# Optimization experiments

Measured on AMD Instinct MI355X. Metric: run time of the kernel, lower is better.

Reference implementation:

```python
import jax, jax.numpy as jnp
import numpy as np

NUM_HEADS = 16

def setup_inputs() -> dict:
    key = jax.random.key(0)
    k1, k2, k3 = jax.random.split(key, 3)
    B, N, D = 2, 2048, 1024
    x = jax.random.normal(k1, (B, N, D), dtype=jnp.float32)
    w_qkv = jax.random.normal(k2, (D, 3 * D), dtype=jnp.float32) * (D ** -0.5)
    w_out = jax.random.normal(k3, (D, D), dtype=jnp.float32) * (D ** -0.5)
    return {"x": x, "w_qkv": w_qkv, "w_out": w_out}

def reference(x, w_qkv, w_out):
    B, N, D = x.shape
    H = NUM_HEADS
    d = D // H
    scale = d ** -0.5
    qkv = x @ w_qkv  # [B, N, 3D]
    q, k, v = jnp.split(qkv, 3, axis=-1)
    # b n (h d) -> b h n d
    split_heads = lambda t: t.reshape(B, N, H, d).transpose(0, 2, 1, 3)
    q, k, v = split_heads(q), split_heads(k), split_heads(v)
    dots = jnp.einsum('bhid,bhjd->bhij', q, k) * scale
    # causal mask: -inf above the diagonal
    causal = jnp.tril(jnp.ones((N, N), dtype=bool))
    dots = jnp.where(causal, dots, jnp.float32(-jnp.inf))
    attn = jax.nn.softmax(dots, axis=-1)
    out = jnp.einsum('bhij,bhjd->bhid', attn, v)
    out = out.transpose(0, 2, 1, 3).reshape(B, N, D)  # b h n d -> b n (h d)
    return out @ w_out
```

## Files before the change

### kernel.cpp

```cpp
#include <hip/hip_runtime.h>


typedef __bf16 bf16x8 __attribute__((ext_vector_type(8)));
typedef float f32x4 __attribute__((ext_vector_type(4)));

#define MFMA16(a, b, c) __builtin_amdgcn_mfma_f32_16x16x32_bf16((a), (b), (c), 0, 0, 0)

#define LDS_FENCE()                                   \
  do {                                                \
    asm volatile("s_waitcnt lgkmcnt(0)" ::: "memory");\
    __builtin_amdgcn_sched_barrier(0);                \
  } while (0)
#define LDS_ORDER() asm volatile("" ::: "memory")

#define MAX3(a, b, c) fmaxf(fmaxf((a), (b)), (c))

__device__ __forceinline__ unsigned short f2bf(float f) {
  __bf16 h = (__bf16)f;
  return *(unsigned short*)&h;
}

__global__ __launch_bounds__(256) void prep_kernel(
    const float* __restrict__ x, const float* __restrict__ wqkv,
    const float* __restrict__ wout, unsigned short* __restrict__ xb,
    unsigned short* __restrict__ wqkvT, unsigned short* __restrict__ woutT) {
  __shared__ float tile[32][33];
  const int id = blockIdx.x, t = threadIdx.x;
  if (id < 4096) {
    const int i = id * 256 + t;
    float4 v = ((const float4*)x)[i];
    ushort4 o;
    o.x = f2bf(v.x); o.y = f2bf(v.y); o.z = f2bf(v.z); o.w = f2bf(v.w);
    ((ushort4*)xb)[i] = o;
    return;
  }
  const int tx = t & 31, ty = t >> 5;
  const float* in; unsigned short* out;
  int C, scale_rows, bx, by;
  if (id < 7168) {
    const int q = id - 4096;
    in = wqkv; out = wqkvT; C = 3072; scale_rows = 1024;
    bx = q % 96; by = q / 96;
  } else {
    const int q = id - 7168;
    in = wout; out = woutT; C = 1024; scale_rows = 0;
    bx = q & 31; by = q >> 5;
  }
#pragma unroll
  for (int i = ty; i < 32; i += 8)
    tile[i][tx] = in[(size_t)(by * 32 + i) * C + bx * 32 + tx];
  __syncthreads();
#pragma unroll
  for (int i = ty; i < 32; i += 8) {
    const int orow = bx * 32 + i;
    const float s = (orow < scale_rows) ? 0.18033688f : 1.0f;
    out[(size_t)orow * 1024 + by * 32 + tx] = f2bf(tile[tx][i] * s);
  }
}

__global__ void transpose_v_kernel(const unsigned short* __restrict__ qkv,
                                   unsigned short* __restrict__ vT) {
  __shared__ unsigned short tile[32][33];
  const int b = blockIdx.z, bx = blockIdx.x, by = blockIdx.y;
  const int tx = threadIdx.x, ty = threadIdx.y;
#pragma unroll
  for (int i = ty; i < 32; i += 8)
    tile[i][tx] = qkv[(size_t)(b * 2048 + by * 32 + i) * 3072 + 2048 + bx * 32 + tx];
  __syncthreads();
#pragma unroll
  for (int i = ty; i < 32; i += 8)
    vT[((size_t)b * 1024 + bx * 32 + i) * 2048 + by * 32 + tx] = tile[tx][i];
}

template <int OUT_BF16>
__global__ __launch_bounds__(256) void gemm128_kernel(
    const unsigned short* __restrict__ A,
    const unsigned short* __restrict__ BT,
    void* __restrict__ Cp, int M, int Nc, int K) {
  __shared__ unsigned short lA[128 * 32];
  __shared__ unsigned short lB[128 * 32];
  const int t = threadIdx.x;
  const int l = t & 63, g = l >> 4, c = l & 15;
  const int w = t >> 6;
  const int wm = (w >> 1) * 64, wn = (w & 1) * 64;
  const int bm = blockIdx.y * 128, bn = blockIdx.x * 128;

  const int i0 = t, i1 = 256 + t;
  const unsigned short* ga0 = A + (size_t)(bm + (i0 >> 2)) * K + (i0 & 3) * 8;
  const unsigned short* ga1 = A + (size_t)(bm + (i1 >> 2)) * K + (i1 & 3) * 8;
  const unsigned short* gb0 = BT + (size_t)(bn + (i0 >> 2)) * K + (i0 & 3) * 8;
  const unsigned short* gb1 = BT + (size_t)(bn + (i1 >> 2)) * K + (i1 & 3) * 8;
  unsigned short* la0 = lA + (i0 & ~63) * 8;
  unsigned short* la1 = lA + (i1 & ~63) * 8;
  unsigned short* lb0 = lB + (i0 & ~63) * 8;
  unsigned short* lb1 = lB + (i1 & ~63) * 8;

  f32x4 acc[4][4] = {};

  for (int kk = 0; kk < K; kk += 32) {
    __syncthreads();
    __builtin_amdgcn_global_load_lds(
        (const __attribute__((address_space(1))) void*)(ga0 + kk),
        (__attribute__((address_space(3))) void*)la0, 16, 0, 0);
    __builtin_amdgcn_global_load_lds(
        (const __attribute__((address_space(1))) void*)(ga1 + kk),
        (__attribute__((address_space(3))) void*)la1, 16, 0, 0);
    __builtin_amdgcn_global_load_lds(
        (const __attribute__((address_space(1))) void*)(gb0 + kk),
        (__attribute__((address_space(3))) void*)lb0, 16, 0, 0);
    __builtin_amdgcn_global_load_lds(
        (const __attribute__((address_space(1))) void*)(gb1 + kk),
        (__attribute__((address_space(3))) void*)lb1, 16, 0, 0);
    __syncthreads();

    bf16x8 af[4], bfr[4];
#pragma unroll
    for (int mi = 0; mi < 4; ++mi)
      af[mi] = *(const bf16x8*)(lA + (wm + mi * 16 + c) * 32 + g * 8);
#pragma unroll
    for (int ni = 0; ni < 4; ++ni)
      bfr[ni] = *(const bf16x8*)(lB + (wn + ni * 16 + c) * 32 + g * 8);
#pragma unroll
    for (int mi = 0; mi < 4; ++mi)
#pragma unroll
      for (int ni = 0; ni < 4; ++ni)
        acc[mi][ni] = MFMA16(af[mi], bfr[ni], acc[mi][ni]);
  }

  if (OUT_BF16) {
    unsigned short* Cc = (unsigned short*)Cp;
#pragma unroll
    for (int mi = 0; mi < 4; ++mi)
#pragma unroll
      for (int r = 0; r < 4; ++r) {
        const int gr = bm + wm + mi * 16 + g * 4 + r;
#pragma unroll
        for (int ni = 0; ni < 4; ++ni)
          Cc[(size_t)gr * Nc + bn + wn + ni * 16 + c] = f2bf(acc[mi][ni][r]);
      }
  } else {
    float* Cf = (float*)Cp;
#pragma unroll
    for (int mi = 0; mi < 4; ++mi)
#pragma unroll
      for (int r = 0; r < 4; ++r) {
        const int gr = bm + wm + mi * 16 + g * 4 + r;
#pragma unroll
        for (int ni = 0; ni < 4; ++ni)
          Cf[(size_t)gr * Nc + bn + wn + ni * 16 + c] = acc[mi][ni][r];
      }
  }
}

__global__ __launch_bounds__(256) void attn_kernel(
    const unsigned short* __restrict__ qkv,
    const unsigned short* __restrict__ vT,
    unsigned short* __restrict__ aout) {
  const int t = threadIdx.x, w = t >> 6, l = t & 63, g = l >> 4, c = l & 15;
  const int g4 = g * 4, c7 = c & 7;

  const int id0 = blockIdx.x;
  const int xcd = id0 & 7, pos = id0 >> 3;
  const int bh = xcd * 4 + (pos & 3);
  const int tile = 31 - (pos >> 2);
  const int b = bh >> 4, h = bh & 15;

  __shared__ __align__(16) unsigned short lK[2][64][64];
  __shared__ __align__(16) unsigned short lV[2][64][64];
  __shared__ __align__(16) unsigned short pl[4][16][40];

  const unsigned short* Qbase = qkv + (size_t)b * 2048 * 3072 + h * 64;
  const unsigned short* Kb = Qbase + 1024;
  const unsigned short* Vb = vT + ((size_t)b * 1024 + h * 64) * 2048;

#define KFRAG(row, half) (*(const bf16x8*)(Kb + (size_t)(row) * 3072 + (half) * 32 + g * 8))
#define VFRAG(dt, kvoff) (*(const bf16x8*)(Vb + (size_t)((dt) * 16 + c) * 2048 + (kvoff) + g * 8))

#define STAGE(dK, dV, kb_)                                                    \
  do {                                                                        \
    _Pragma("unroll")                                                         \
    for (int q = 0; q < 2; ++q) {                                             \
      const int idx = q * 256 + t;                                            \
      const int row = idx >> 3, ch = idx & 7;                                 \
      const int sc = (ch ^ (row & 7)) * 8;                                    \
      __builtin_amdgcn_global_load_lds(                                       \
          (const __attribute__((address_space(1))) void*)(                    \
              Kb + (size_t)(kb_ + row) * 3072 + sc),                          \
          (__attribute__((address_space(3))) void*)(                          \
              &(dK)[0][0] + (idx & ~63) * 8), 16, 0, 0);                      \
      __builtin_amdgcn_global_load_lds(                                       \
          (const __attribute__((address_space(1))) void*)(                    \
              Vb + (size_t)row * 2048 + (kb_) + sc),                          \
          (__attribute__((address_space(3))) void*)(                          \
              &(dV)[0][0] + (idx & ~63) * 8), 16, 0, 0);                      \
    }                                                                         \
  } while (0)

  const int q0 = tile * 64 + w * 16;
  const int qc = q0 + c;

  const bf16x8 bq0 = *(const bf16x8*)(Qbase + (size_t)qc * 3072 + g * 8);
  const bf16x8 bq1 = *(const bf16x8*)(Qbase + (size_t)qc * 3072 + 32 + g * 8);

  f32x4 o[4] = {};
  float m_c = -__builtin_inff(), llp = 0.f;

  if (tile > 0) {
    STAGE(lK[0], lV[0], 0);
    int cur = 0;
#pragma unroll 1
    for (int jb = 0; jb < tile; ++jb) {
      __syncthreads();
      if (jb + 1 < tile) STAGE(lK[cur ^ 1], lV[cur ^ 1], (jb + 1) * 64);

      const unsigned short* lk = &lK[cur][0][0];
      const unsigned short* lv = &lV[cur][0][0];

      bf16x8 ka[8];
#pragma unroll
      for (int n = 0; n < 4; ++n) {
        ka[2 * n]     = *(const bf16x8*)(lk + (16 * n + c) * 64 + ((g ^ c7) * 8));
        ka[2 * n + 1] = *(const bf16x8*)(lk + (16 * n + c) * 64 + (((4 + g) ^ c7) * 8));
      }
      bf16x8 bv[2][4];
#pragma unroll
      for (int ks = 0; ks < 2; ++ks)
#pragma unroll
        for (int dt = 0; dt < 4; ++dt)
          bv[ks][dt] = *(const bf16x8*)(lv + (dt * 16 + c) * 64 + (((ks * 4 + g) ^ c7) * 8));

      f32x4 s[4] = {};
      __builtin_amdgcn_s_setprio(1);
#pragma unroll
      for (int n = 0; n < 4; ++n) {
        s[n] = MFMA16(ka[2 * n], bq0, s[n]);
        s[n] = MFMA16(ka[2 * n + 1], bq1, s[n]);
      }
      __builtin_amdgcn_s_setprio(0);

      const float t0 = MAX3(s[0][0], s[0][1], s[0][2]);
      const float t1 = MAX3(s[0][3], s[1][0], s[1][1]);
      const float t2 = MAX3(s[1][2], s[1][3], s[2][0]);
      const float t3 = MAX3(s[2][1], s[2][2], s[2][3]);
      const float t4 = MAX3(s[3][0], s[3][1], s[3][2]);
      const float vml = fmaxf(MAX3(t0, t1, t2), MAX3(t3, t4, s[3][3]));

      if (!__all(vml - m_c <= 5.0f)) {
        float vm = vml;
        vm = fmaxf(vm, __shfl_xor(vm, 16));
        vm = fmaxf(vm, __shfl_xor(vm, 32));
        const float mn = fmaxf(m_c, vm);
        const float al = exp2f(m_c - mn);
        m_c = mn;
        llp *= al;
#pragma unroll
        for (int r = 0; r < 4; ++r) {
          const float alr = __shfl(al, g4 + r);
          o[0][r] *= alr; o[1][r] *= alr; o[2][r] *= alr; o[3][r] *= alr;
        }
      }

#pragma unroll
      for (int n = 0; n < 4; ++n)
#pragma unroll
        for (int r = 0; r < 4; ++r)
          s[n][r] = exp2f(s[n][r] - m_c);

      llp += ((s[0][0] + s[0][1]) + (s[0][2] + s[0][3])) +
             ((s[1][0] + s[1][1]) + (s[1][2] + s[1][3])) +
             ((s[2][0] + s[2][1]) + (s[2][2] + s[2][3])) +
             ((s[3][0] + s[3][1]) + (s[3][2] + s[3][3]));

      LDS_ORDER();
#pragma unroll
      for (int n = 0; n < 2; ++n) {
        ushort4 pw;
        pw.x = f2bf(s[n][0]); pw.y = f2bf(s[n][1]);
        pw.z = f2bf(s[n][2]); pw.w = f2bf(s[n][3]);
        *(ushort4*)&pl[w][c][n * 16 + g4] = pw;
      }
      LDS_FENCE();
      const bf16x8 pa0 = *(const bf16x8*)&pl[w][c][g * 8];
      LDS_FENCE();
#pragma unroll
      for (int n = 2; n < 4; ++n) {
        ushort4 pw;
        pw.x = f2bf(s[n][0]); pw.y = f2bf(s[n][1]);
        pw.z = f2bf(s[n][2]); pw.w = f2bf(s[n][3]);
        *(ushort4*)&pl[w][c][(n - 2) * 16 + g4] = pw;
      }
      LDS_FENCE();
      const bf16x8 pa1 = *(const bf16x8*)&pl[w][c][g * 8];

      __builtin_amdgcn_s_setprio(1);
#pragma unroll
      for (int dt = 0; dt < 4; ++dt) {
        o[dt] = MFMA16(pa0, bv[0][dt], o[dt]);
        o[dt] = MFMA16(pa1, bv[1][dt], o[dt]);
      }
      __builtin_amdgcn_s_setprio(0);
      cur ^= 1;
    }
  }

  const int ndiag = 1 + (w >> 1);
#pragma unroll 1
  for (int j = 0; j < ndiag; ++j) {
    const int kb = tile * 64 + j * 32;
    const bf16x8 k00 = KFRAG(kb + c, 0), k01 = KFRAG(kb + c, 1);
    const bf16x8 k10 = KFRAG(kb + 16 + c, 0), k11 = KFRAG(kb + 16 + c, 1);
    const bf16x8 bv0 = VFRAG(0, kb), bv1 = VFRAG(1, kb);
    const bf16x8 bv2 = VFRAG(2, kb), bv3 = VFRAG(3, kb);

    f32x4 s0 = {}, s1 = {};
    s0 = MFMA16(k00, bq0, s0);
    s0 = MFMA16(k01, bq1, s0);
    s1 = MFMA16(k10, bq0, s1);
    s1 = MFMA16(k11, bq1, s1);

    float v0[4], v1[4];
#pragma unroll
    for (int r = 0; r < 4; ++r) {
      v0[r] = (kb + g4 + r <= qc) ? s0[r] : -__builtin_inff();
      v1[r] = (kb + 16 + g4 + r <= qc) ? s1[r] : -__builtin_inff();
    }
    const float t0 = MAX3(v0[0], v0[1], v0[2]);
    const float t1 = MAX3(v0[3], v1[0], v1[1]);
    const float vml = fmaxf(fmaxf(t0, t1), fmaxf(v1[2], v1[3]));
    if (!__all(vml - m_c <= 5.0f)) {
      float vm = vml;
      vm = fmaxf(vm, __shfl_xor(vm, 16));
      vm = fmaxf(vm, __shfl_xor(vm, 32));
      const float mn = fmaxf(m_c, vm);
      const float al = exp2f(m_c - mn);
      m_c = mn;
      llp *= al;
#pragma unroll
      for (int r = 0; r < 4; ++r) {
        const float alr = __shfl(al, g4 + r);
        o[0][r] *= alr; o[1][r] *= alr; o[2][r] *= alr; o[3][r] *= alr;
      }
    }
    float p0[4], p1[4];
#pragma unroll
    for (int r = 0; r < 4; ++r) {
      p0[r] = exp2f(v0[r] - m_c);
      p1[r] = exp2f(v1[r] - m_c);
    }
    llp += ((p0[0] + p0[1]) + (p0[2] + p0[3])) +
           ((p1[0] + p1[1]) + (p1[2] + p1[3]));

    LDS_ORDER();
    ushort4 pw;
    pw.x = f2bf(p0[0]); pw.y = f2bf(p0[1]); pw.z = f2bf(p0[2]); pw.w = f2bf(p0[3]);
    *(ushort4*)&pl[w][c][g4] = pw;
    pw.x = f2bf(p1[0]); pw.y = f2bf(p1[1]); pw.z = f2bf(p1[2]); pw.w = f2bf(p1[3]);
    *(ushort4*)&pl[w][c][16 + g4] = pw;
    LDS_FENCE();
    const bf16x8 pa = *(const bf16x8*)&pl[w][c][g * 8];

    o[0] = MFMA16(pa, bv0, o[0]);
    o[1] = MFMA16(pa, bv1, o[1]);
    o[2] = MFMA16(pa, bv2, o[2]);
    o[3] = MFMA16(pa, bv3, o[3]);
  }

  float ll = llp;
  ll += __shfl_xor(ll, 16);
  ll += __shfl_xor(ll, 32);
  const float inv = 1.0f / ll;
#pragma unroll
  for (int r = 0; r < 4; ++r) {
    const float invr = __shfl(inv, g4 + r);
    const size_t row = (size_t)(b * 2048 + q0 + g4 + r);
#pragma unroll
    for (int dt = 0; dt < 4; ++dt)
      aout[row * 1024 + h * 64 + dt * 16 + c] = f2bf(o[dt][r] * invr);
  }
#undef KFRAG
#undef VFRAG
#undef STAGE
}

extern "C" void kernel_launch(void* const* d_in, const int* in_sizes, int n_in,
                              void* d_out, int out_size, void* d_ws, size_t ws_size,
                              hipStream_t stream) {
  const float* x = (const float*)d_in[0];
  const float* wqkv = (const float*)d_in[1];
  const float* wout = (const float*)d_in[2];
  float* out = (float*)d_out;

  unsigned short* ws = (unsigned short*)d_ws;
  unsigned short* xb = ws;
  unsigned short* wqkvT = xb + (size_t)4096 * 1024;
  unsigned short* woutT = wqkvT + (size_t)3072 * 1024;
  unsigned short* qkv = woutT + (size_t)1024 * 1024;
  unsigned short* vT = qkv + (size_t)4096 * 3072;
  unsigned short* aout = vT + (size_t)2 * 1024 * 2048;

  prep_kernel<<<8192, 256, 0, stream>>>(x, wqkv, wout, xb, wqkvT, woutT);
  gemm128_kernel<1><<<dim3(24, 32), 256, 0, stream>>>(xb, wqkvT, qkv, 4096, 3072, 1024);
  transpose_v_kernel<<<dim3(32, 64, 2), dim3(32, 8), 0, stream>>>(qkv, vT);
  attn_kernel<<<1024, 256, 0, stream>>>(qkv, vT, aout);
  gemm128_kernel<0><<<dim3(8, 32), 256, 0, stream>>>(aout, woutT, out, 4096, 1024, 1024);
}
```

Measured before the change: 132.8 us.

## Switch attention to 32x32 MFMA with register-shuffled P fragments and 2-wave blocks

Rewrites the attention kernel to use 32x32x16 bf16 MFMA tiles, with each of two waves per block owning 32 query rows instead of four waves owning 16. The P matrix is converted to bf16 with packed conversions and rearranged through cross-lane shuffles rather than a round trip through LDS with wait fences. The diagonal blocks are also handled per wave with 32-wide chunks. This cuts LDS traffic and synchronisation for P and raises MFMA efficiency, but it halves the threads per block, doubles per-thread accumulator and register pressure, and doubles each thread's staging load share.

Result: slower. 152.7 us (+15.0%).

```diff
diff --git a/kernel.cpp b/kernel.cpp
--- a/kernel.cpp
+++ b/kernel.cpp
@@ -3,22 +3,36 @@
 
 typedef __bf16 bf16x8 __attribute__((ext_vector_type(8)));
 typedef float f32x4 __attribute__((ext_vector_type(4)));
+typedef float f32x16 __attribute__((ext_vector_type(16)));
+typedef unsigned int uint4v __attribute__((ext_vector_type(4)));
 
 #define MFMA16(a, b, c) __builtin_amdgcn_mfma_f32_16x16x32_bf16((a), (b), (c), 0, 0, 0)
-
-#define LDS_FENCE()                                   \
-  do {                                                \
-    asm volatile("s_waitcnt lgkmcnt(0)" ::: "memory");\
-    __builtin_amdgcn_sched_barrier(0);                \
-  } while (0)
-#define LDS_ORDER() asm volatile("" ::: "memory")
-
-#define MAX3(a, b, c) fmaxf(fmaxf((a), (b)), (c))
+#define MFMA32(a, b, c) __builtin_amdgcn_mfma_f32_32x32x16_bf16((a), (b), (c), 0, 0, 0)
 
 __device__ __forceinline__ unsigned short f2bf(float f) {
   __bf16 h = (__bf16)f;
   return *(unsigned short*)&h;
 }
+
+__device__ __forceinline__ unsigned cvtpk_bf16(float lo, float hi) {
+  unsigned r;
+  asm("v_cvt_pk_bf16_f32 %0, %1, %2" : "=v"(r) : "v"(lo), "v"(hi));
+  return r;
+}
+
+#define PFRAG(dst, sv, base)                                   \
+  do {                                                         \
+    const unsigned X0 = cvtpk_bf16((sv)[(base) + 0], (sv)[(base) + 1]); \
+    const unsigned X1 = cvtpk_bf16((sv)[(base) + 2], (sv)[(base) + 3]); \
+    const unsigned Y0 = cvtpk_bf16((sv)[(base) + 4], (sv)[(base) + 5]); \
+    const unsigned Y1 = cvtpk_bf16((sv)[(base) + 6], (sv)[(base) + 7]); \
+    const unsigned c0 = __shfl_xor(hi ? X0 : Y0, 32);          \
+    const unsigned c1 = __shfl_xor(hi ? X1 : Y1, 32);          \
+    uint4v u;                                                  \
+    u.x = hi ? c0 : X0; u.y = hi ? c1 : X1;                    \
+    u.z = hi ? Y0 : c0; u.w = hi ? Y1 : c1;                    \
+    dst = __builtin_bit_cast(bf16x8, u);                       \
+  } while (0)
 
 __global__ __launch_bounds__(256) void prep_kernel(
     const float* __restrict__ x, const float* __restrict__ wqkv,
@@ -152,35 +166,36 @@
   }
 }
 
-__global__ __launch_bounds__(256) void attn_kernel(
+__global__ __launch_bounds__(128, 2) void attn_kernel(
     const unsigned short* __restrict__ qkv,
     const unsigned short* __restrict__ vT,
     unsigned short* __restrict__ aout) {
-  const int t = threadIdx.x, w = t >> 6, l = t & 63, g = l >> 4, c = l & 15;
-  const int g4 = g * 4, c7 = c & 7;
+  const int t = threadIdx.x;
+  const int w = t >> 6;
+  const int l = t & 63;
+  const int col = l & 31;
+  const int hi = l >> 5;
+  const int hi4 = hi * 4;
+  const int c7 = col & 7;
 
   const int id0 = blockIdx.x;
   const int xcd = id0 & 7, pos = id0 >> 3;
   const int bh = xcd * 4 + (pos & 3);
-  const int tile = 31 - (pos >> 2);
+  const int T = 31 - (pos >> 2);
   const int b = bh >> 4, h = bh & 15;
 
   __shared__ __align__(16) unsigned short lK[2][64][64];
   __shared__ __align__(16) unsigned short lV[2][64][64];
-  __shared__ __align__(16) unsigned short pl[4][16][40];
 
   const unsigned short* Qbase = qkv + (size_t)b * 2048 * 3072 + h * 64;
   const unsigned short* Kb = Qbase + 1024;
   const unsigned short* Vb = vT + ((size_t)b * 1024 + h * 64) * 2048;
 
-#define KFRAG(row, half) (*(const bf16x8*)(Kb + (size_t)(row) * 3072 + (half) * 32 + g * 8))
-#define VFRAG(dt, kvoff) (*(const bf16x8*)(Vb + (size_t)((dt) * 16 + c) * 2048 + (kvoff) + g * 8))
-
 #define STAGE(dK, dV, kb_)                                                    \
   do {                                                                        \
     _Pragma("unroll")                                                         \
-    for (int q = 0; q < 2; ++q) {                                             \
-      const int idx = q * 256 + t;                                            \
+    for (int qq = 0; qq < 4; ++qq) {                                          \
+      const int idx = qq * 128 + t;                                           \
       const int row = idx >> 3, ch = idx & 7;                                 \
       const int sc = (ch ^ (row & 7)) * 8;                                    \
       __builtin_amdgcn_global_load_lds(                                       \
@@ -196,189 +211,165 @@
     }                                                                         \
   } while (0)
 
-  const int q0 = tile * 64 + w * 16;
-  const int qc = q0 + c;
-
-  const bf16x8 bq0 = *(const bf16x8*)(Qbase + (size_t)qc * 3072 + g * 8);
-  const bf16x8 bq1 = *(const bf16x8*)(Qbase + (size_t)qc * 3072 + 32 + g * 8);
-
-  f32x4 o[4] = {};
+  const int q0w = T * 64 + w * 32;
+  const int qg = q0w + col;
+
+  bf16x8 bq[4];
+#pragma unroll
+  for (int c16 = 0; c16 < 4; ++c16)
+    bq[c16] = *(const bf16x8*)(Qbase + (size_t)qg * 3072 + c16 * 16 + hi * 8);
+
+  f32x16 o0 = {}, o1 = {};
   float m_c = -__builtin_inff(), llp = 0.f;
 
-  if (tile > 0) {
+  if (T > 0) {
     STAGE(lK[0], lV[0], 0);
     int cur = 0;
 #pragma unroll 1
-    for (int jb = 0; jb < tile; ++jb) {
+    for (int jb = 0; jb < T; ++jb) {
       __syncthreads();
-      if (jb + 1 < tile) STAGE(lK[cur ^ 1], lV[cur ^ 1], (jb + 1) * 64);
+      if (jb + 1 < T) STAGE(lK[cur ^ 1], lV[cur ^ 1], (jb + 1) * 64);
 
       const unsigned short* lk = &lK[cur][0][0];
       const unsigned short* lv = &lV[cur][0][0];
 
-      bf16x8 ka[8];
-#pragma unroll
-      for (int n = 0; n < 4; ++n) {
-        ka[2 * n]     = *(const bf16x8*)(lk + (16 * n + c) * 64 + ((g ^ c7) * 8));
-        ka[2 * n + 1] = *(const bf16x8*)(lk + (16 * n + c) * 64 + (((4 + g) ^ c7) * 8));
-      }
-      bf16x8 bv[2][4];
-#pragma unroll
-      for (int ks = 0; ks < 2; ++ks)
-#pragma unroll
-        for (int dt = 0; dt < 4; ++dt)
-          bv[ks][dt] = *(const bf16x8*)(lv + (dt * 16 + c) * 64 + (((ks * 4 + g) ^ c7) * 8));
-
-      f32x4 s[4] = {};
+      f32x16 s0 = {}, s1 = {};
       __builtin_amdgcn_s_setprio(1);
 #pragma unroll
-      for (int n = 0; n < 4; ++n) {
-        s[n] = MFMA16(ka[2 * n], bq0, s[n]);
-        s[n] = MFMA16(ka[2 * n + 1], bq1, s[n]);
+      for (int c16 = 0; c16 < 4; ++c16) {
+        const int chl = c16 * 2 + hi;
+        const bf16x8 k0 = *(const bf16x8*)(lk + (col)*64 + ((chl ^ c7) * 8));
+        const bf16x8 k1 = *(const bf16x8*)(lk + (32 + col) * 64 + ((chl ^ c7) * 8));
+        s0 = MFMA32(k0, bq[c16], s0);
+        s1 = MFMA32(k1, bq[c16], s1);
       }
       __builtin_amdgcn_s_setprio(0);
 
-      const float t0 = MAX3(s[0][0], s[0][1], s[0][2]);
-      const float t1 = MAX3(s[0][3], s[1][0], s[1][1]);
-      const float t2 = MAX3(s[1][2], s[1][3], s[2][0]);
-      const float t3 = MAX3(s[2][1], s[2][2], s[2][3]);
-      const float t4 = MAX3(s[3][0], s[3][1], s[3][2]);
-      const float vml = fmaxf(MAX3(t0, t1, t2), MAX3(t3, t4, s[3][3]));
+      float a[16];
+#pragma unroll
+      for (int i = 0; i < 16; ++i) a[i] = fmaxf(s0[i], s1[i]);
+#pragma unroll
+      for (int kk = 8; kk; kk >>= 1)
+#pragma unroll
+        for (int i = 0; i < kk; ++i) a[i] = fmaxf(a[i], a[i + kk]);
+      const float vml = fmaxf(a[0], __shfl_xor(a[0], 32));
 
       if (!__all(vml - m_c <= 5.0f)) {
-        float vm = vml;
-        vm = fmaxf(vm, __shfl_xor(vm, 16));
-        vm = fmaxf(vm, __shfl_xor(vm, 32));
-        const float mn = fmaxf(m_c, vm);
+        const float mn = fmaxf(m_c, vml);
         const float al = exp2f(m_c - mn);
-        m_c = mn;
-        llp *= al;
-#pragma unroll
-        for (int r = 0; r < 4; ++r) {
-          const float alr = __shfl(al, g4 + r);
-          o[0][r] *= alr; o[1][r] *= alr; o[2][r] *= alr; o[3][r] *= alr;
+        m_c = mn; llp *= al;
+#pragma unroll
+        for (int r = 0; r < 16; ++r) {
+          const float alr = __shfl(al, (r & 3) + 8 * (r >> 2) + hi4);
+          o0[r] *= alr; o1[r] *= alr;
         }
       }
 
 #pragma unroll
-      for (int n = 0; n < 4; ++n)
-#pragma unroll
-        for (int r = 0; r < 4; ++r)
-          s[n][r] = exp2f(s[n][r] - m_c);
-
-      llp += ((s[0][0] + s[0][1]) + (s[0][2] + s[0][3])) +
-             ((s[1][0] + s[1][1]) + (s[1][2] + s[1][3])) +
-             ((s[2][0] + s[2][1]) + (s[2][2] + s[2][3])) +
-             ((s[3][0] + s[3][1]) + (s[3][2] + s[3][3]));
-
-      LDS_ORDER();
-#pragma unroll
-      for (int n = 0; n < 2; ++n) {
-        ushort4 pw;
-        pw.x = f2bf(s[n][0]); pw.y = f2bf(s[n][1]);
-        pw.z = f2bf(s[n][2]); pw.w = f2bf(s[n][3]);
-        *(ushort4*)&pl[w][c][n * 16 + g4] = pw;
-      }
-      LDS_FENCE();
-      const bf16x8 pa0 = *(const bf16x8*)&pl[w][c][g * 8];
-      LDS_FENCE();
-#pragma unroll
-      for (int n = 2; n < 4; ++n) {
-        ushort4 pw;
-        pw.x = f2bf(s[n][0]); pw.y = f2bf(s[n][1]);
-        pw.z = f2bf(s[n][2]); pw.w = f2bf(s[n][3]);
-        *(ushort4*)&pl[w][c][(n - 2) * 16 + g4] = pw;
-      }
-      LDS_FENCE();
-      const bf16x8 pa1 = *(const bf16x8*)&pl[w][c][g * 8];
+      for (int i = 0; i < 16; ++i) {
+        s0[i] = exp2f(s0[i] - m_c);
+        s1[i] = exp2f(s1[i] - m_c);
+      }
+      float sm[16];
+#pragma unroll
+      for (int i = 0; i < 16; ++i) sm[i] = s0[i] + s1[i];
+#pragma unroll
+      for (int kk = 8; kk; kk >>= 1)
+#pragma unroll
+        for (int i = 0; i < kk; ++i) sm[i] += sm[i + kk];
+      llp += sm[0];
+
+      bf16x8 pf0, pf1, pf2, pf3;
+      PFRAG(pf0, s0, 0); PFRAG(pf1, s0, 8);
+      PFRAG(pf2, s1, 0); PFRAG(pf3, s1, 8);
 
       __builtin_amdgcn_s_setprio(1);
 #pragma unroll
-      for (int dt = 0; dt < 4; ++dt) {
-        o[dt] = MFMA16(pa0, bv[0][dt], o[dt]);
-        o[dt] = MFMA16(pa1, bv[1][dt], o[dt]);
+      for (int ck = 0; ck < 4; ++ck) {
+        const int chl = ck * 2 + hi;
+        const bf16x8 v0 = *(const bf16x8*)(lv + (col)*64 + ((chl ^ c7) * 8));
+        const bf16x8 v1 = *(const bf16x8*)(lv + (32 + col) * 64 + ((chl ^ c7) * 8));
+        const bf16x8 pf = (ck == 0) ? pf0 : (ck == 1) ? pf1 : (ck == 2) ? pf2 : pf3;
+        o0 = MFMA32(pf, v0, o0);
+        o1 = MFMA32(pf, v1, o1);
       }
       __builtin_amdgcn_s_setprio(0);
       cur ^= 1;
     }
   }
 
-  const int ndiag = 1 + (w >> 1);
-#pragma unroll 1
-  for (int j = 0; j < ndiag; ++j) {
-    const int kb = tile * 64 + j * 32;
-    const bf16x8 k00 = KFRAG(kb + c, 0), k01 = KFRAG(kb + c, 1);
-    const bf16x8 k10 = KFRAG(kb + 16 + c, 0), k11 = KFRAG(kb + 16 + c, 1);
-    const bf16x8 bv0 = VFRAG(0, kb), bv1 = VFRAG(1, kb);
-    const bf16x8 bv2 = VFRAG(2, kb), bv3 = VFRAG(3, kb);
-
-    f32x4 s0 = {}, s1 = {};
-    s0 = MFMA16(k00, bq0, s0);
-    s0 = MFMA16(k01, bq1, s0);
-    s1 = MFMA16(k10, bq0, s1);
-    s1 = MFMA16(k11, bq1, s1);
-
-    float v0[4], v1[4];
-#pragma unroll
-    for (int r = 0; r < 4; ++r) {
-      v0[r] = (kb + g4 + r <= qc) ? s0[r] : -__builtin_inff();
-      v1[r] = (kb + 16 + g4 + r <= qc) ? s1[r] : -__builtin_inff();
-    }
-    const float t0 = MAX3(v0[0], v0[1], v0[2]);
-    const float t1 = MAX3(v0[3], v1[0], v1[1]);
-    const float vml = fmaxf(fmaxf(t0, t1), fmaxf(v1[2], v1[3]));
+  for (int j = 0; j <= w; ++j) {
+    const int kb = T * 64 + j * 32;
+    const bool masked = (j == w);
+
+    f32x16 s = {};
+#pragma unroll
+    for (int c16 = 0; c16 < 4; ++c16) {
+      const bf16x8 kf = *(const bf16x8*)(Kb + (size_t)(kb + col) * 3072 + c16 * 16 + hi * 8);
+      s = MFMA32(kf, bq[c16], s);
+    }
+
+    if (masked) {
+#pragma unroll
+      for (int r = 0; r < 16; ++r) {
+        const int kvg = kb + (r & 3) + 8 * (r >> 2) + hi4;
+        s[r] = (kvg <= qg) ? s[r] : -__builtin_inff();
+      }
+    }
+
+    float a[16];
+#pragma unroll
+    for (int i = 0; i < 16; ++i) a[i] = s[i];
+#pragma unroll
+    for (int kk = 8; kk; kk >>= 1)
+#pragma unroll
+      for (int i = 0; i < kk; ++i) a[i] = fmaxf(a[i], a[i + kk]);
+    const float vml = fmaxf(a[0], __shfl_xor(a[0], 32));
+
     if (!__all(vml - m_c <= 5.0f)) {
-      float vm = vml;
-      vm = fmaxf(vm, __shfl_xor(vm, 16));
-      vm = fmaxf(vm, __shfl_xor(vm, 32));
-      const float mn = fmaxf(m_c, vm);
+      const float mn = fmaxf(m_c, vml);
       const float al = exp2f(m_c - mn);
-      m_c = mn;
-      llp *= al;
-#pragma unroll
-      for (int r = 0; r < 4; ++r) {
-        const float alr = __shfl(al, g4 + r);
-        o[0][r] *= alr; o[1][r] *= alr; o[2][r] *= alr; o[3][r] *= alr;
-      }
-    }
-    float p0[4], p1[4];
-#pragma unroll
-    for (int r = 0; r < 4; ++r) {
-      p0[r] = exp2f(v0[r] - m_c);
-      p1[r] = exp2f(v1[r] - m_c);
-    }
-    llp += ((p0[0] + p0[1]) + (p0[2] + p0[3])) +
-           ((p1[0] + p1[1]) + (p1[2] + p1[3]));
-
-    LDS_ORDER();
-    ushort4 pw;
-    pw.x = f2bf(p0[0]); pw.y = f2bf(p0[1]); pw.z = f2bf(p0[2]); pw.w = f2bf(p0[3]);
-    *(ushort4*)&pl[w][c][g4] = pw;
-    pw.x = f2bf(p1[0]); pw.y = f2bf(p1[1]); pw.z = f2bf(p1[2]); pw.w = f2bf(p1[3]);
-    *(ushort4*)&pl[w][c][16 + g4] = pw;
-    LDS_FENCE();
-    const bf16x8 pa = *(const bf16x8*)&pl[w][c][g * 8];
-
-    o[0] = MFMA16(pa, bv0, o[0]);
-    o[1] = MFMA16(pa, bv1, o[1]);
-    o[2] = MFMA16(pa, bv2, o[2]);
-    o[3] = MFMA16(pa, bv3, o[3]);
-  }
-
-  float ll = llp;
-  ll += __shfl_xor(ll, 16);
-  ll += __shfl_xor(ll, 32);
+      m_c = mn; llp *= al;
+#pragma unroll
+      for (int r = 0; r < 16; ++r) {
+        const float alr = __shfl(al, (r & 3) + 8 * (r >> 2) + hi4);
+        o0[r] *= alr; o1[r] *= alr;
+      }
+    }
+
+#pragma unroll
+    for (int i = 0; i < 16; ++i) s[i] = exp2f(s[i] - m_c);
+    float sm[16];
+#pragma unroll
+    for (int i = 0; i < 16; ++i) sm[i] = s[i];
+#pragma unroll
+    for (int kk = 8; kk; kk >>= 1)
+#pragma unroll
+      for (int i = 0; i < kk; ++i) sm[i] += sm[i + kk];
+    llp += sm[0];
+
+    bf16x8 pf0, pf1;
+    PFRAG(pf0, s, 0); PFRAG(pf1, s, 8);
+#pragma unroll
+    for (int ck = 0; ck < 2; ++ck) {
+      const bf16x8 v0 = *(const bf16x8*)(Vb + (size_t)(col)*2048 + kb + ck * 16 + hi * 8);
+      const bf16x8 v1 = *(const bf16x8*)(Vb + (size_t)(32 + col) * 2048 + kb + ck * 16 + hi * 8);
+      const bf16x8 pf = ck ? pf1 : pf0;
+      o0 = MFMA32(pf, v0, o0);
+      o1 = MFMA32(pf, v1, o1);
+    }
+  }
+
+  const float ll = llp + __shfl_xor(llp, 32);
   const float inv = 1.0f / ll;
 #pragma unroll
-  for (int r = 0; r < 4; ++r) {
-    const float invr = __shfl(inv, g4 + r);
-    const size_t row = (size_t)(b * 2048 + q0 + g4 + r);
-#pragma unroll
-    for (int dt = 0; dt < 4; ++dt)
-      aout[row * 1024 + h * 64 + dt * 16 + c] = f2bf(o[dt][r] * invr);
-  }
-#undef KFRAG
-#undef VFRAG
+  for (int r = 0; r < 16; ++r) {
+    const int qrow = (r & 3) + 8 * (r >> 2) + hi4;
+    const float invr = __shfl(inv, qrow);
+    const size_t row = (size_t)(b * 2048 + q0w + qrow);
+    aout[row * 1024 + h * 64 + col] = f2bf(o0[r] * invr);
+    aout[row * 1024 + h * 64 + 32 + col] = f2bf(o1[r] * invr);
+  }
 #undef STAGE
 }
 
@@ -401,6 +392,6 @@
   prep_kernel<<<8192, 256, 0, stream>>>(x, wqkv, wout, xb, wqkvT, woutT);
   gemm128_kernel<1><<<dim3(24, 32), 256, 0, stream>>>(xb, wqkvT, qkv, 4096, 3072, 1024);
   transpose_v_kernel<<<dim3(32, 64, 2), dim3(32, 8), 0, stream>>>(qkv, vT);
-  attn_kernel<<<1024, 256, 0, stream>>>(qkv, vT, aout);
+  attn_kernel<<<1024, 128, 0, stream>>>(qkv, vT, aout);
   gemm128_kernel<0><<<dim3(8, 32), 256, 0, stream>>>(aout, woutT, out, 4096, 1024, 1024);
 }
```

## Fuse V transpose into QKV GEMM epilogue and add XCD-aware block swizzle

Applied to the files above, without the earlier changes.

The QKV GEMM now writes the V slice directly in transposed layout from its epilogue, which removes the separate transpose kernel launch and its extra read and write of V. Both GEMMs use a 1D grid with an XCD-aware swizzle of block indices, aiming for better L2 locality. In the attention kernel the P staging buffer is widened so all four score tiles are written with one fence instead of two write/read rounds. The s_setprio hints and the max3 reductions are dropped. The transposed V stores are 8-byte writes strided by 2048 elements, so they may coalesce poorly.

New measurement: 123.1 us. -7.3%, faster.

```diff
diff --git a/kernel.cpp b/kernel.cpp
--- a/kernel.cpp
+++ b/kernel.cpp
@@ -11,9 +11,6 @@
     asm volatile("s_waitcnt lgkmcnt(0)" ::: "memory");\
     __builtin_amdgcn_sched_barrier(0);                \
   } while (0)
-#define LDS_ORDER() asm volatile("" ::: "memory")
-
-#define MAX3(a, b, c) fmaxf(fmaxf((a), (b)), (c))
 
 __device__ __forceinline__ unsigned short f2bf(float f) {
   __bf16 h = (__bf16)f;
@@ -58,32 +55,23 @@
   }
 }
 
-__global__ void transpose_v_kernel(const unsigned short* __restrict__ qkv,
-                                   unsigned short* __restrict__ vT) {
-  __shared__ unsigned short tile[32][33];
-  const int b = blockIdx.z, bx = blockIdx.x, by = blockIdx.y;
-  const int tx = threadIdx.x, ty = threadIdx.y;
-#pragma unroll
-  for (int i = ty; i < 32; i += 8)
-    tile[i][tx] = qkv[(size_t)(b * 2048 + by * 32 + i) * 3072 + 2048 + bx * 32 + tx];
-  __syncthreads();
-#pragma unroll
-  for (int i = ty; i < 32; i += 8)
-    vT[((size_t)b * 1024 + bx * 32 + i) * 2048 + by * 32 + tx] = tile[tx][i];
-}
-
-template <int OUT_BF16>
+template <int MODE>
 __global__ __launch_bounds__(256) void gemm128_kernel(
     const unsigned short* __restrict__ A,
     const unsigned short* __restrict__ BT,
-    void* __restrict__ Cp, int M, int Nc, int K) {
+    void* __restrict__ Cp, unsigned short* __restrict__ vTp,
+    int M, int Nc, int K, int NX) {
+  const int id0 = blockIdx.x;
+  const int swz = (id0 & 7) * ((int)gridDim.x >> 3) + (id0 >> 3);
+  const int bx = swz % NX, by = swz / NX;
+
   __shared__ unsigned short lA[128 * 32];
   __shared__ unsigned short lB[128 * 32];
   const int t = threadIdx.x;
   const int l = t & 63, g = l >> 4, c = l & 15;
   const int w = t >> 6;
   const int wm = (w >> 1) * 64, wn = (w & 1) * 64;
-  const int bm = blockIdx.y * 128, bn = blockIdx.x * 128;
+  const int bm = by * 128, bn = bx * 128;
 
   const int i0 = t, i1 = 256 + t;
   const unsigned short* ga0 = A + (size_t)(bm + (i0 >> 2)) * K + (i0 & 3) * 8;
@@ -127,8 +115,8 @@
         acc[mi][ni] = MFMA16(af[mi], bfr[ni], acc[mi][ni]);
   }
 
-  if (OUT_BF16) {
-    unsigned short* Cc = (unsigned short*)Cp;
+  if (MODE == 0) {
+    float* Cf = (float*)Cp;
 #pragma unroll
     for (int mi = 0; mi < 4; ++mi)
 #pragma unroll
@@ -136,10 +124,24 @@
         const int gr = bm + wm + mi * 16 + g * 4 + r;
 #pragma unroll
         for (int ni = 0; ni < 4; ++ni)
-          Cc[(size_t)gr * Nc + bn + wn + ni * 16 + c] = f2bf(acc[mi][ni][r]);
+          Cf[(size_t)gr * Nc + bn + wn + ni * 16 + c] = acc[mi][ni][r];
+      }
+  } else if (MODE == 2 && bn >= 2048) {
+    const int bq = bm >> 11;
+    const int nbase = bm - bq * 2048 + wm;
+#pragma unroll
+    for (int mi = 0; mi < 4; ++mi)
+#pragma unroll
+      for (int ni = 0; ni < 4; ++ni) {
+        const int dimg = bn - 2048 + wn + ni * 16 + c;
+        ushort4 pk;
+        pk.x = f2bf(acc[mi][ni][0]); pk.y = f2bf(acc[mi][ni][1]);
+        pk.z = f2bf(acc[mi][ni][2]); pk.w = f2bf(acc[mi][ni][3]);
+        *(ushort4*)(vTp + ((size_t)(bq * 1024 + dimg)) * 2048 + nbase +
+                    mi * 16 + g * 4) = pk;
       }
   } else {
-    float* Cf = (float*)Cp;
+    unsigned short* Cc = (unsigned short*)Cp;
 #pragma unroll
     for (int mi = 0; mi < 4; ++mi)
 #pragma unroll
@@ -147,7 +149,7 @@
         const int gr = bm + wm + mi * 16 + g * 4 + r;
 #pragma unroll
         for (int ni = 0; ni < 4; ++ni)
-          Cf[(size_t)gr * Nc + bn + wn + ni * 16 + c] = acc[mi][ni][r];
+          Cc[(size_t)gr * Nc + bn + wn + ni * 16 + c] = f2bf(acc[mi][ni][r]);
       }
   }
 }
@@ -167,7 +169,7 @@
 
   __shared__ __align__(16) unsigned short lK[2][64][64];
   __shared__ __align__(16) unsigned short lV[2][64][64];
-  __shared__ __align__(16) unsigned short pl[4][16][40];
+  __shared__ __align__(16) unsigned short pl[4][16][72];
 
   const unsigned short* Qbase = qkv + (size_t)b * 2048 * 3072 + h * 64;
   const unsigned short* Kb = Qbase + 1024;
@@ -230,20 +232,17 @@
           bv[ks][dt] = *(const bf16x8*)(lv + (dt * 16 + c) * 64 + (((ks * 4 + g) ^ c7) * 8));
 
       f32x4 s[4] = {};
-      __builtin_amdgcn_s_setprio(1);
 #pragma unroll
       for (int n = 0; n < 4; ++n) {
         s[n] = MFMA16(ka[2 * n], bq0, s[n]);
         s[n] = MFMA16(ka[2 * n + 1], bq1, s[n]);
       }
-      __builtin_amdgcn_s_setprio(0);
-
-      const float t0 = MAX3(s[0][0], s[0][1], s[0][2]);
-      const float t1 = MAX3(s[0][3], s[1][0], s[1][1]);
-      const float t2 = MAX3(s[1][2], s[1][3], s[2][0]);
-      const float t3 = MAX3(s[2][1], s[2][2], s[2][3]);
-      const float t4 = MAX3(s[3][0], s[3][1], s[3][2]);
-      const float vml = fmaxf(MAX3(t0, t1, t2), MAX3(t3, t4, s[3][3]));
+
+      float m01 = fmaxf(fmaxf(s[0][0], s[0][1]), fmaxf(s[0][2], s[0][3]));
+      float m23 = fmaxf(fmaxf(s[1][0], s[1][1]), fmaxf(s[1][2], s[1][3]));
+      float m45 = fmaxf(fmaxf(s[2][0], s[2][1]), fmaxf(s[2][2], s[2][3]));
+      float m67 = fmaxf(fmaxf(s[3][0], s[3][1]), fmaxf(s[3][2], s[3][3]));
+      const float vml = fmaxf(fmaxf(m01, m23), fmaxf(m45, m67));
 
       if (!__all(vml - m_c <= 5.0f)) {
         float vm = vml;
@@ -271,9 +270,9 @@
              ((s[2][0] + s[2][1]) + (s[2][2] + s[2][3])) +
              ((s[3][0] + s[3][1]) + (s[3][2] + s[3][3]));
 
-      LDS_ORDER();
-#pragma unroll
-      for (int n = 0; n < 2; ++n) {
+      LDS_FENCE();
+#pragma unroll
+      for (int n = 0; n < 4; ++n) {
         ushort4 pw;
         pw.x = f2bf(s[n][0]); pw.y = f2bf(s[n][1]);
         pw.z = f2bf(s[n][2]); pw.w = f2bf(s[n][3]);
@@ -281,24 +280,13 @@
       }
       LDS_FENCE();
       const bf16x8 pa0 = *(const bf16x8*)&pl[w][c][g * 8];
-      LDS_FENCE();
-#pragma unroll
-      for (int n = 2; n < 4; ++n) {
-        ushort4 pw;
-        pw.x = f2bf(s[n][0]); pw.y = f2bf(s[n][1]);
-        pw.z = f2bf(s[n][2]); pw.w = f2bf(s[n][3]);
-        *(ushort4*)&pl[w][c][(n - 2) * 16 + g4] = pw;
-      }
-      LDS_FENCE();
-      const bf16x8 pa1 = *(const bf16x8*)&pl[w][c][g * 8];
-
-      __builtin_amdgcn_s_setprio(1);
+      const bf16x8 pa1 = *(const bf16x8*)&pl[w][c][32 + g * 8];
+
 #pragma unroll
       for (int dt = 0; dt < 4; ++dt) {
         o[dt] = MFMA16(pa0, bv[0][dt], o[dt]);
         o[dt] = MFMA16(pa1, bv[1][dt], o[dt]);
       }
-      __builtin_amdgcn_s_setprio(0);
       cur ^= 1;
     }
   }
@@ -324,9 +312,8 @@
       v0[r] = (kb + g4 + r <= qc) ? s0[r] : -__builtin_inff();
       v1[r] = (kb + 16 + g4 + r <= qc) ? s1[r] : -__builtin_inff();
     }
-    const float t0 = MAX3(v0[0], v0[1], v0[2]);
-    const float t1 = MAX3(v0[3], v1[0], v1[1]);
-    const float vml = fmaxf(fmaxf(t0, t1), fmaxf(v1[2], v1[3]));
+    const float vml = fmaxf(fmaxf(fmaxf(v0[0], v0[1]), fmaxf(v0[2], v0[3])),
+                            fmaxf(fmaxf(v1[0], v1[1]), fmaxf(v1[2], v1[3])));
     if (!__all(vml - m_c <= 5.0f)) {
       float vm = vml;
       vm = fmaxf(vm, __shfl_xor(vm, 16));
@@ -350,7 +337,7 @@
     llp += ((p0[0] + p0[1]) + (p0[2] + p0[3])) +
            ((p1[0] + p1[1]) + (p1[2] + p1[3]));
 
-    LDS_ORDER();
+    LDS_FENCE();
     ushort4 pw;
     pw.x = f2bf(p0[0]); pw.y = f2bf(p0[1]); pw.z = f2bf(p0[2]); pw.w = f2bf(p0[3]);
     *(ushort4*)&pl[w][c][g4] = pw;
@@ -399,8 +386,7 @@
   unsigned short* aout = vT + (size_t)2 * 1024 * 2048;
 
   prep_kernel<<<8192, 256, 0, stream>>>(x, wqkv, wout, xb, wqkvT, woutT);
-  gemm128_kernel<1><<<dim3(24, 32), 256, 0, stream>>>(xb, wqkvT, qkv, 4096, 3072, 1024);
-  transpose_v_kernel<<<dim3(32, 64, 2), dim3(32, 8), 0, stream>>>(qkv, vT);
+  gemm128_kernel<2><<<768, 256, 0, stream>>>(xb, wqkvT, qkv, vT, 4096, 3072, 1024, 24);
   attn_kernel<<<1024, 256, 0, stream>>>(qkv, vT, aout);
-  gemm128_kernel<0><<<dim3(8, 32), 256, 0, stream>>>(aout, woutT, out, 4096, 1024, 1024);
-}
+  gemm128_kernel<0><<<256, 256, 0, stream>>>(aout, woutT, out, nullptr, 4096, 1024, 1024, 8);
+}
```
